# Kernel tuning notes

Hardware: AMD Instinct MI355X
Metric: run time of the kernel (lower is better)

The kernel has to match this reference:

```python
import jax, jax.numpy as jnp
import numpy as np
import math

B, S, D, H, L, V = 1, 2048, 512, 8, 2, 32000
DH = D // H
DFF = 2048
EPS = 1e-6
LN_EPS = 1e-5


def setup_inputs() -> dict:
    key = jax.random.key(0)
    ks = jax.random.split(key, 8)
    s = 0.02
    return {
        "input_ids": jax.random.randint(ks[0], (B, S), 0, V),
        "token_emb": jax.random.normal(ks[1], (V, D), jnp.float32) * s,
        "ln1_scale": jnp.ones((L, D), jnp.float32),
        "ln1_bias": jnp.zeros((L, D), jnp.float32),
        "qkv_w": jax.random.normal(ks[2], (L, D, 3 * D), jnp.float32) * s,
        "out_w": jax.random.normal(ks[3], (L, D, D), jnp.float32) * s,
        "ln2_scale": jnp.ones((L, D), jnp.float32),
        "ln2_bias": jnp.zeros((L, D), jnp.float32),
        "mlp_w1": jax.random.normal(ks[4], (L, D, DFF), jnp.float32) * s,
        "mlp_b1": jnp.zeros((L, DFF), jnp.float32),
        "mlp_w2": jax.random.normal(ks[5], (L, DFF, D), jnp.float32) * s,
        "mlp_b2": jnp.zeros((L, D), jnp.float32),
        "lnf_scale": jnp.ones((D,), jnp.float32),
        "lnf_bias": jnp.zeros((D,), jnp.float32),
        "head_w": jax.random.normal(ks[6], (D, V), jnp.float32) * s,
    }


def layernorm(x, scale, bias):
    mu = jnp.mean(x, axis=-1, keepdims=True)
    var = jnp.mean(jnp.square(x - mu), axis=-1, keepdims=True)
    return (x - mu) * jax.lax.rsqrt(var + LN_EPS) * scale + bias


def feature_map(x):
    return jax.nn.elu(x) + 1.0


def sinusoidal_pe(seq_len, d_model, dtype):
    pos = jnp.arange(seq_len, dtype=jnp.float32)[:, None]
    div = jnp.exp(jnp.arange(0, d_model, 2, dtype=jnp.float32) * (-math.log(10000.0) / d_model))
    pe = jnp.zeros((seq_len, d_model), jnp.float32)
    pe = pe.at[:, 0::2].set(jnp.sin(pos * div))
    pe = pe.at[:, 1::2].set(jnp.cos(pos * div))
    return pe.astype(dtype)


def linear_causal_attn(x, w_qkv, w_out):
    # x: (b, s, d)
    b, s, _ = x.shape
    qkv = x @ w_qkv  # (b, s, 3d)
    q, k, v = jnp.split(qkv, 3, axis=-1)
    split_heads = lambda t: t.reshape(b, s, H, DH).transpose(0, 2, 1, 3)  # (b,h,s,dh)
    q, k, v = split_heads(q), split_heads(k), split_heads(v)
    phi_q = feature_map(q)
    phi_k = feature_map(k)
    k_cum = jnp.cumsum(phi_k, axis=2)                          # (b,h,s,dh)
    kv = jnp.einsum('bhsi,bhsj->bhsij', phi_k, v)              # (b,h,s,dh,dh)
    kv_cum = jnp.cumsum(kv, axis=2)
    numer = jnp.einsum('bhsi,bhsij->bhsj', phi_q, kv_cum)      # (b,h,s,dh)
    denom = jnp.einsum('bhsi,bhsi->bhs', phi_q, k_cum) + EPS
    attn = numer / denom[..., None]
    attn = attn.transpose(0, 2, 1, 3).reshape(b, s, D)
    return attn @ w_out


def reference(input_ids, token_emb, ln1_scale, ln1_bias, qkv_w, out_w,
              ln2_scale, ln2_bias, mlp_w1, mlp_b1, mlp_w2, mlp_b2,
              lnf_scale, lnf_bias, head_w):
    tok = token_emb[input_ids]                 # (b, s, d)
    pos = sinusoidal_pe(input_ids.shape[1], D, tok.dtype)[None]
    x = tok + pos
    for l in range(L):
        a = linear_causal_attn(layernorm(x, ln1_scale[l], ln1_bias[l]), qkv_w[l], out_w[l])
        x = x + a
        h = layernorm(x, ln2_scale[l], ln2_bias[l])
        h = jax.nn.gelu(h @ mlp_w1[l] + mlp_b1[l], approximate=False) @ mlp_w2[l] + mlp_b2[l]
        x = x + h
    x = layernorm(x, lnf_scale, lnf_bias)
    logits = x @ head_w                        # (b, s, vocab)
    return logits
```

## Files before the change

### kernel.cpp

```cpp
#include <hip/hip_runtime.h>
#include <cstdint>

typedef unsigned short u16;
typedef __bf16 bf16x8 __attribute__((ext_vector_type(8)));
typedef float f32x4 __attribute__((ext_vector_type(4)));

#define DEV __device__ __forceinline__

DEV u16 f2bf(float f) {
  union { float f; unsigned u; } v; v.f = f;
  unsigned u = v.u;
  u += 0x7FFFu + ((u >> 16) & 1u);
  return (u16)(u >> 16);
}
DEV float bf2f(u16 u) {
  union { unsigned u; float f; } v; v.u = ((unsigned)u) << 16;
  return v.f;
}

DEV void load16(const u16* g, u16* l) {
  __builtin_amdgcn_global_load_lds(
      (const __attribute__((address_space(1))) unsigned int*)(const void*)g,
      (__attribute__((address_space(3))) unsigned int*)l, 16, 0, 0);
}

__global__ __launch_bounds__(256) void prep_kernel(
    const float* __restrict__ qkvw, const float* __restrict__ outw,
    const float* __restrict__ w1, const float* __restrict__ w2,
    const float* __restrict__ hw, u16* __restrict__ wq_t, u16* __restrict__ wo_t,
    u16* __restrict__ w1_t, u16* __restrict__ w2_t, u16* __restrict__ wh_t,
    const int* __restrict__ ids, const float* __restrict__ emb,
    const float* __restrict__ sc, const float* __restrict__ bi,
    float* __restrict__ x, u16* __restrict__ xn) {
  int b = blockIdx.x;
  __shared__ float t[64][65];
  if (b >= 5536) {
    int lane = threadIdx.x & 63, wave = threadIdx.x >> 6;
    int row = (b - 5536) * 4 + wave;
    int id = ids[row];
    float v[8];
#pragma unroll
    for (int i = 0; i < 8; ++i) {
      int c = lane + i * 64;
      float tk = emb[(size_t)id * 512 + c];
      int dp = c & ~1;
      float dv = expf((float)dp * (-9.210340371976184f / 512.0f));
      float ang = (float)row * dv;
      float pe = (c & 1) ? cosf(ang) : sinf(ang);
      v[i] = tk + pe;
      x[(size_t)row * 512 + c] = v[i];
    }
    float s = 0.f;
#pragma unroll
    for (int i = 0; i < 8; ++i) s += v[i];
#pragma unroll
    for (int m = 32; m; m >>= 1) s += __shfl_xor(s, m, 64);
    float mu = s * (1.0f / 512.0f);
    float var = 0.f;
#pragma unroll
    for (int i = 0; i < 8; ++i) { float d = v[i] - mu; var += d * d; }
#pragma unroll
    for (int m = 32; m; m >>= 1) var += __shfl_xor(var, m, 64);
    float rs = rsqrtf(var * (1.0f / 512.0f) + 1e-5f);
    u16* orow = xn + (size_t)row * 512;
#pragma unroll
    for (int i = 0; i < 8; ++i) {
      int c = lane + i * 64;
      orow[c] = f2bf((v[i] - mu) * rs * sc[c] + bi[c]);
    }
    return;
  }
  const float* in; u16* out; int K, N, nx, ky;
  if (b < 384)       { int z = b / 192, r = b % 192; nx = r % 24; ky = r / 24;
                       in = qkvw + (size_t)z * 786432; out = wq_t + (size_t)z * 786432; N = 1536; K = 512; }
  else if (b < 512)  { int tt = b - 384, z = tt / 64, r = tt % 64; nx = r % 8; ky = r / 8;
                       in = outw + (size_t)z * 262144; out = wo_t + (size_t)z * 262144; N = 512; K = 512; }
  else if (b < 1024) { int tt = b - 512, z = tt / 256, r = tt % 256; nx = r % 32; ky = r / 32;
                       in = w1 + (size_t)z * 1048576; out = w1_t + (size_t)z * 1048576; N = 2048; K = 512; }
  else if (b < 1536) { int tt = b - 1024, z = tt / 256, r = tt % 256; nx = r % 8; ky = r / 8;
                       in = w2 + (size_t)z * 1048576; out = w2_t + (size_t)z * 1048576; N = 512; K = 2048; }
  else               { int tt = b - 1536; nx = tt % 500; ky = tt / 500;
                       in = hw; out = wh_t; N = 32000; K = 512; }
  int n0 = nx * 64, k0 = ky * 64;
  for (int e = threadIdx.x; e < 4096; e += 256) {
    int r = e >> 6, c = e & 63;
    t[r][c] = in[(size_t)(k0 + r) * N + n0 + c];
  }
  __syncthreads();
  for (int e = threadIdx.x; e < 4096; e += 256) {
    int r = e >> 6, c = e & 63;
    out[(size_t)(n0 + r) * K + k0 + c] = f2bf(t[c][r]);
  }
}

__global__ __launch_bounds__(256) void reduce_ln(const float* __restrict__ part, int nz,
    const float* __restrict__ bias, float* __restrict__ x,
    const float* __restrict__ sc, const float* __restrict__ bi, u16* __restrict__ xn) {
  int lane = threadIdx.x & 63, wave = threadIdx.x >> 6;
  int row = blockIdx.x * 4 + wave;
  float* xr = x + (size_t)row * 512;
  float v[8];
#pragma unroll
  for (int i = 0; i < 8; ++i) v[i] = xr[lane + i * 64];
  if (bias) {
#pragma unroll
    for (int i = 0; i < 8; ++i) v[i] += bias[lane + i * 64];
  }
  for (int z = 0; z < nz; ++z) {
    const float* pz = part + (size_t)z * 1048576 + (size_t)row * 512;
#pragma unroll
    for (int i = 0; i < 8; ++i) v[i] += pz[lane + i * 64];
  }
#pragma unroll
  for (int i = 0; i < 8; ++i) xr[lane + i * 64] = v[i];
  float s = 0.f;
#pragma unroll
  for (int i = 0; i < 8; ++i) s += v[i];
#pragma unroll
  for (int m = 32; m; m >>= 1) s += __shfl_xor(s, m, 64);
  float mu = s * (1.0f / 512.0f);
  float var = 0.f;
#pragma unroll
  for (int i = 0; i < 8; ++i) { float d = v[i] - mu; var += d * d; }
#pragma unroll
  for (int m = 32; m; m >>= 1) var += __shfl_xor(var, m, 64);
  float rs = rsqrtf(var * (1.0f / 512.0f) + 1e-5f);
  u16* orow = xn + (size_t)row * 512;
#pragma unroll
  for (int i = 0; i < 8; ++i) {
    int c = lane + i * 64;
    orow[c] = f2bf((v[i] - mu) * rs * sc[c] + bi[c]);
  }
}

__global__ __launch_bounds__(256) void attn_intra(const u16* __restrict__ pq,
    const u16* __restrict__ pk, const u16* __restrict__ pv,
    float* __restrict__ numer, float* __restrict__ denom,
    float* __restrict__ KVc, float* __restrict__ Ksc) {
  int c = blockIdx.x, h = blockIdx.y;
  int s0 = c * 128;
  __shared__ u16 kl[128 * 72];
  __shared__ u16 kT[64 * 136];
  __shared__ u16 vT[64 * 136];
  __shared__ u16 P[128 * 136];
  int tid = threadIdx.x, lane = tid & 63, w = tid >> 6;
  int fr = lane & 15, kb = lane >> 4, rg = lane >> 4;
  const size_t base = ((size_t)h * 2048 + s0) * 64;

  for (int e = tid; e < 1024; e += 256) {
    int r = e >> 3, c8 = (e & 7) * 8;
    bf16x8 kv = *(const bf16x8*)&pk[base + r * 64 + c8];
    bf16x8 vv = *(const bf16x8*)&pv[base + r * 64 + c8];
    *(bf16x8*)&kl[r * 72 + c8] = kv;
#pragma unroll
    for (int tt = 0; tt < 8; ++tt) {
      kT[(c8 + tt) * 136 + r] = ((const u16*)&kv)[tt];
      vT[(c8 + tt) * 136 + r] = ((const u16*)&vv)[tt];
    }
  }
  int fiA = w, fiB = 7 - w;
  const u16* qA = pq + base + (size_t)(fiA * 16 + fr) * 64 + kb * 8;
  const u16* qB = pq + base + (size_t)(fiB * 16 + fr) * 64 + kb * 8;
  bf16x8 aQ0a = *(const bf16x8*)qA, aQ1a = *(const bf16x8*)(qA + 32);
  bf16x8 aQ0b = *(const bf16x8*)qB, aQ1b = *(const bf16x8*)(qB + 32);
  __syncthreads();

#pragma unroll
  for (int ph = 0; ph < 2; ++ph) {
    int fi = ph ? fiB : fiA;
    bf16x8 aQ0 = ph ? aQ0b : aQ0a, aQ1 = ph ? aQ1b : aQ1a;
    f32x4 dsum = {0.f, 0.f, 0.f, 0.f};
    for (int fj = 0; fj <= fi; ++fj) {
      f32x4 s4 = {0.f, 0.f, 0.f, 0.f};
      bf16x8 b0 = *(const bf16x8*)&kl[(fj * 16 + fr) * 72 + kb * 8];
      bf16x8 b1 = *(const bf16x8*)&kl[(fj * 16 + fr) * 72 + kb * 8 + 32];
      s4 = __builtin_amdgcn_mfma_f32_16x16x32_bf16(aQ0, b0, s4, 0, 0, 0);
      s4 = __builtin_amdgcn_mfma_f32_16x16x32_bf16(aQ1, b1, s4, 0, 0, 0);
      int colL = fj * 16 + fr;
#pragma unroll
      for (int rr = 0; rr < 4; ++rr) {
        int rowL = fi * 16 + rg * 4 + rr;
        float mv = (colL <= rowL) ? s4[rr] : 0.f;
        dsum[rr] += mv;
        P[rowL * 136 + colL] = f2bf(mv);
      }
    }
    if ((fi & 1) == 0) {
      int colL = (fi + 1) * 16 + fr;
#pragma unroll
      for (int rr = 0; rr < 4; ++rr) P[(fi * 16 + rg * 4 + rr) * 136 + colL] = 0;
    }
#pragma unroll
    for (int rr = 0; rr < 4; ++rr) {
      float v = dsum[rr];
      v += __shfl_xor(v, 1, 16); v += __shfl_xor(v, 2, 16);
      v += __shfl_xor(v, 4, 16); v += __shfl_xor(v, 8, 16);
      if (fr == 0) denom[(size_t)h * 2048 + s0 + fi * 16 + rg * 4 + rr] = v;
    }
  }
  __syncthreads();

#pragma unroll
  for (int ph = 0; ph < 2; ++ph) {
    int fi = ph ? fiB : fiA;
    int ktmax = (fi + 2) >> 1;
    f32x4 o0 = {0,0,0,0}, o1 = {0,0,0,0}, o2 = {0,0,0,0}, o3 = {0,0,0,0};
    for (int kt = 0; kt < ktmax; ++kt) {
      bf16x8 aP = *(const bf16x8*)&P[(fi * 16 + fr) * 136 + kt * 32 + kb * 8];
      o0 = __builtin_amdgcn_mfma_f32_16x16x32_bf16(aP, *(const bf16x8*)&vT[(0 * 16 + fr) * 136 + kt * 32 + kb * 8], o0, 0, 0, 0);
      o1 = __builtin_amdgcn_mfma_f32_16x16x32_bf16(aP, *(const bf16x8*)&vT[(1 * 16 + fr) * 136 + kt * 32 + kb * 8], o1, 0, 0, 0);
      o2 = __builtin_amdgcn_mfma_f32_16x16x32_bf16(aP, *(const bf16x8*)&vT[(2 * 16 + fr) * 136 + kt * 32 + kb * 8], o2, 0, 0, 0);
      o3 = __builtin_amdgcn_mfma_f32_16x16x32_bf16(aP, *(const bf16x8*)&vT[(3 * 16 + fr) * 136 + kt * 32 + kb * 8], o3, 0, 0, 0);
    }
#pragma unroll
    for (int rr = 0; rr < 4; ++rr) {
      size_t rb = base + (size_t)(fi * 16 + rg * 4 + rr) * 64;
      numer[rb + 0 + fr]  = o0[rr];
      numer[rb + 16 + fr] = o1[rr];
      numer[rb + 32 + fr] = o2[rr];
      numer[rb + 48 + fr] = o3[rr];
    }
  }

  {
    f32x4 k0 = {0,0,0,0}, k1 = {0,0,0,0}, k2 = {0,0,0,0}, k3 = {0,0,0,0};
    for (int kt = 0; kt < 4; ++kt) {
      bf16x8 aK = *(const bf16x8*)&kT[(w * 16 + fr) * 136 + kt * 32 + kb * 8];
      k0 = __builtin_amdgcn_mfma_f32_16x16x32_bf16(aK, *(const bf16x8*)&vT[(0 * 16 + fr) * 136 + kt * 32 + kb * 8], k0, 0, 0, 0);
      k1 = __builtin_amdgcn_mfma_f32_16x16x32_bf16(aK, *(const bf16x8*)&vT[(1 * 16 + fr) * 136 + kt * 32 + kb * 8], k1, 0, 0, 0);
      k2 = __builtin_amdgcn_mfma_f32_16x16x32_bf16(aK, *(const bf16x8*)&vT[(2 * 16 + fr) * 136 + kt * 32 + kb * 8], k2, 0, 0, 0);
      k3 = __builtin_amdgcn_mfma_f32_16x16x32_bf16(aK, *(const bf16x8*)&vT[(3 * 16 + fr) * 136 + kt * 32 + kb * 8], k3, 0, 0, 0);
    }
    float* kvb = KVc + ((size_t)h * 16 + c) * 4096;
#pragma unroll
    for (int rr = 0; rr < 4; ++rr) {
      int row = w * 16 + rg * 4 + rr;
      kvb[row * 64 + 0 + fr]  = k0[rr];
      kvb[row * 64 + 16 + fr] = k1[rr];
      kvb[row * 64 + 32 + fr] = k2[rr];
      kvb[row * 64 + 48 + fr] = k3[rr];
    }
  }
  if (tid < 64) {
    float s = 0.f;
    for (int t8 = 0; t8 < 16; ++t8) {
      bf16x8 kv = *(const bf16x8*)&kT[tid * 136 + t8 * 8];
#pragma unroll
      for (int tt = 0; tt < 8; ++tt) s += bf2f(((const u16*)&kv)[tt]);
    }
    Ksc[((size_t)h * 16 + c) * 64 + tid] = s;
  }
}

__global__ __launch_bounds__(256) void attn_inter(const u16* __restrict__ pq,
    const float* __restrict__ numer, const float* __restrict__ denom,
    const float* __restrict__ KVc, const float* __restrict__ Ksc,
    u16* __restrict__ attn) {
  int c = blockIdx.x, h = blockIdx.y;
  int s0 = c * 128;
  __shared__ float KVp[4096];
  __shared__ float Kp[64];
  __shared__ float ql[128 * 64];
  int tid = threadIdx.x;
  for (int e = tid; e < 1024; e += 256) {
    f32x4 a = {0.f, 0.f, 0.f, 0.f};
    for (int cp = 0; cp < c; ++cp)
      a += *(const f32x4*)&KVc[((size_t)h * 16 + cp) * 4096 + e * 4];
    *(f32x4*)&KVp[e * 4] = a;
  }
  if (tid < 64) {
    float a = 0.f;
    for (int cp = 0; cp < c; ++cp) a += Ksc[((size_t)h * 16 + cp) * 64 + tid];
    Kp[tid] = a;
  }
  for (int e = tid; e < 1024; e += 256) {
    bf16x8 q8 = *(const bf16x8*)&pq[((size_t)h * 2048 + s0) * 64 + e * 8];
#pragma unroll
    for (int tt = 0; tt < 8; ++tt) ql[e * 8 + tt] = bf2f(((const u16*)&q8)[tt]);
  }
  __syncthreads();
  int s = tid >> 1, half = tid & 1;
  float num[32];
  {
    const float* np_ = numer + ((size_t)h * 2048 + s0 + s) * 64 + half * 32;
#pragma unroll
    for (int i = 0; i < 8; ++i) *(f32x4*)&num[i * 4] = *(const f32x4*)&np_[i * 4];
  }
  float den = denom[(size_t)h * 2048 + s0 + s] + 1e-6f;
  for (int i = 0; i < 64; ++i) {
    float qv = ql[s * 64 + i];
    den += qv * Kp[i];
    const f32x4* kv = (const f32x4*)&KVp[i * 64 + half * 32];
#pragma unroll
    for (int j4 = 0; j4 < 8; ++j4) {
      f32x4 kvv = kv[j4];
#pragma unroll
      for (int t = 0; t < 4; ++t) num[j4 * 4 + t] += qv * kvv[t];
    }
  }
  float inv = 1.f / den;
  u16* op = attn + (size_t)(s0 + s) * 512 + h * 64 + half * 32;
#pragma unroll
  for (int j = 0; j < 32; ++j) op[j] = f2bf(num[j] * inv);
}

template <int EPI>
__global__ __launch_bounds__(512, 2) void gemm_bt(const u16* __restrict__ A,
    const u16* __restrict__ B, float* __restrict__ outF, u16* __restrict__ outB,
    const float* __restrict__ bias, int M, int N, int K, int Ksplit) {
  __shared__ u16 lds[32768];
  int tid = threadIdx.x, lane = tid & 63, w = tid >> 6;
  int f = blockIdx.x + gridDim.x * blockIdx.y;
  int m0 = (f & 15) << 7, n0 = (f >> 4) << 7;
  int wr = w >> 2, wc = w & 3;
  int fr = lane & 15, kb = lane >> 4;
  int z = blockIdx.z;
  int kbeg = z * Ksplit;
  int KT = Ksplit >> 6;

  auto stage = [&](int d, int u, int k0) {
    int t = u & 1;
    int row = t * 64 + w * 8 + (lane >> 3);
    int slot = (lane & 7) ^ ((lane >> 3) & 7);
    const u16* g = (u < 2 ? A + (size_t)(m0 + row) * K : B + (size_t)(n0 + row) * K)
                   + k0 + slot * 8;
    int dst = (u < 2 ? d * 8192 : 16384 + d * 8192) + t * 4096 + w * 512;
    load16(g, &lds[dst]);
  };
  auto rdA = [&](int d, int i, int kk) {
    int row = wr * 64 + i * 16 + fr;
    return *(const bf16x8*)&lds[d * 8192 + row * 64 + ((((kk << 2) | kb) ^ (fr & 7)) << 3)];
  };
  auto rdB = [&](int d, int j, int kk) {
    int row = wc * 32 + j * 16 + fr;
    return *(const bf16x8*)&lds[16384 + d * 8192 + row * 64 + ((((kk << 2) | kb) ^ (fr & 7)) << 3)];
  };

  f32x4 acc[4][2];
#pragma unroll
  for (int i = 0; i < 4; ++i)
#pragma unroll
    for (int j = 0; j < 2; ++j) acc[i][j] = (f32x4){0.f, 0.f, 0.f, 0.f};

#pragma unroll 1
  for (int u = 0; u < 4; ++u) stage(0, u, kbeg);
  __syncthreads();

  for (int t = 0; t < KT; ++t) {
    int d = t & 1, e = d ^ 1;
    int k1 = kbeg + ((t + 1) << 6);
    bool pre = (t + 1) < KT;
    bf16x8 aF[4], bF[2];
    if (pre) { stage(e, 0, k1); stage(e, 1, k1); }
#pragma unroll
    for (int i = 0; i < 4; ++i) aF[i] = rdA(d, i, 0);
#pragma unroll
    for (int j = 0; j < 2; ++j) bF[j] = rdB(d, j, 0);
    __builtin_amdgcn_s_setprio(1);
#pragma unroll
    for (int i = 0; i < 4; ++i)
#pragma unroll
      for (int j = 0; j < 2; ++j)
        acc[i][j] = __builtin_amdgcn_mfma_f32_16x16x32_bf16(aF[i], bF[j], acc[i][j], 0, 0, 0);
    __builtin_amdgcn_s_setprio(0);
    __builtin_amdgcn_sched_barrier(0);
    if (pre) { stage(e, 2, k1); stage(e, 3, k1); }
#pragma unroll
    for (int i = 0; i < 4; ++i) aF[i] = rdA(d, i, 1);
#pragma unroll
    for (int j = 0; j < 2; ++j) bF[j] = rdB(d, j, 1);
    __builtin_amdgcn_s_setprio(1);
#pragma unroll
    for (int i = 0; i < 4; ++i)
#pragma unroll
      for (int j = 0; j < 2; ++j)
        acc[i][j] = __builtin_amdgcn_mfma_f32_16x16x32_bf16(aF[i], bF[j], acc[i][j], 0, 0, 0);
    __builtin_amdgcn_s_setprio(0);
    __syncthreads();
  }

  int rq = lane >> 4;
#pragma unroll
  for (int i = 0; i < 4; ++i) {
#pragma unroll
    for (int j = 0; j < 2; ++j) {
      int col = n0 + wc * 32 + j * 16 + fr;
#pragma unroll
      for (int r = 0; r < 4; ++r) {
        int row = m0 + wr * 64 + i * 16 + rq * 4 + r;
        size_t o = (size_t)row * N + col;
        float vacc = acc[i][j][r];
        if (EPI == 2) {
          float t = vacc + bias[col];
          outB[o] = f2bf(0.5f * t * (1.f + erff(t * 0.70710678118654752f)));
        } else if (EPI == 4) {
          int part = col >> 9, d = col & 511, h = d >> 6, dh = d & 63;
          float wv = (part == 2) ? vacc : (vacc > 0.f ? vacc + 1.f : expf(vacc));
          outB[(size_t)part * 1048576 + (((size_t)h * 2048 + row) * 64 + dh)] = f2bf(wv);
        } else {
          outF[(size_t)z * 1048576 + o] = vacc;
        }
      }
    }
  }
}

__global__ __launch_bounds__(512, 2) void gemm256(const u16* __restrict__ A,
    const u16* __restrict__ B, float* __restrict__ C, int M, int N, int K) {
  __shared__ u16 lds[65536];
  int tid = threadIdx.x, lane = tid & 63, w = tid >> 6;
  int f = blockIdx.x;
  {
    int nwg = gridDim.x;
    int q = nwg >> 3;
    f = (f & 7) * q + (f >> 3);
  }
  int m0 = (f & 7) << 8;
  int n0 = (f >> 3) << 8;
  int wr = w >> 2, wc = w & 3;
  int fr = lane & 15, kb = lane >> 4;

  auto stage = [&](int d, int u, int k0) {
    int us = u & 3;
    int row = us * 64 + w * 8 + (lane >> 3);
    int slot = (lane & 7) ^ ((lane >> 3) & 7);
    const u16* g = (u < 4 ? A + (size_t)(m0 + row) * K : B + (size_t)(n0 + row) * K)
                   + k0 + slot * 8;
    int dst = (u < 4 ? d * 16384 : 32768 + d * 16384) + us * 4096 + w * 512;
    load16(g, &lds[dst]);
  };
  auto rdA = [&](int d, int i, int kk) {
    int row = wr * 128 + i * 16 + fr;
    return *(const bf16x8*)&lds[d * 16384 + row * 64 + ((((kk << 2) | kb) ^ (fr & 7)) << 3)];
  };
  auto rdB = [&](int d, int j, int kk) {
    int row = wc * 64 + j * 16 + fr;
    return *(const bf16x8*)&lds[32768 + d * 16384 + row * 64 + ((((kk << 2) | kb) ^ (fr & 7)) << 3)];
  };

  f32x4 acc[8][4];
#pragma unroll
  for (int i = 0; i < 8; ++i)
#pragma unroll
    for (int j = 0; j < 4; ++j) acc[i][j] = (f32x4){0.f, 0.f, 0.f, 0.f};

  int KT = K >> 6;
#pragma unroll 1
  for (int u = 0; u < 8; ++u) stage(0, u, 0);
  __syncthreads();

  for (int t = 0; t < KT; ++t) {
    int d = t & 1, e = d ^ 1;
    int k1 = (t + 1) << 6;
    bool pre = (t + 1) < KT;
    bf16x8 aF[4][2], bF[4][2];
    if (pre) { stage(e, 0, k1); stage(e, 1, k1); }
#pragma unroll
    for (int i = 0; i < 4; ++i) { aF[i][0] = rdA(d, i, 0); aF[i][1] = rdA(d, i, 1); }
#pragma unroll
    for (int j = 0; j < 2; ++j) { bF[j][0] = rdB(d, j, 0); bF[j][1] = rdB(d, j, 1); }
    __builtin_amdgcn_s_setprio(1);
#pragma unroll
    for (int i = 0; i < 4; ++i)
#pragma unroll
      for (int j = 0; j < 2; ++j)
#pragma unroll
        for (int kk = 0; kk < 2; ++kk)
          acc[i][j] = __builtin_amdgcn_mfma_f32_16x16x32_bf16(aF[i][kk], bF[j][kk], acc[i][j], 0, 0, 0);
    __builtin_amdgcn_s_setprio(0);
    __builtin_amdgcn_sched_barrier(0);
    if (pre) { stage(e, 2, k1); stage(e, 3, k1); }
#pragma unroll
    for (int j = 2; j < 4; ++j) { bF[j][0] = rdB(d, j, 0); bF[j][1] = rdB(d, j, 1); }
    __builtin_amdgcn_s_setprio(1);
#pragma unroll
    for (int i = 0; i < 4; ++i)
#pragma unroll
      for (int j = 2; j < 4; ++j)
#pragma unroll
        for (int kk = 0; kk < 2; ++kk)
          acc[i][j] = __builtin_amdgcn_mfma_f32_16x16x32_bf16(aF[i][kk], bF[j][kk], acc[i][j], 0, 0, 0);
    __builtin_amdgcn_s_setprio(0);
    __builtin_amdgcn_sched_barrier(0);
    if (pre) { stage(e, 4, k1); stage(e, 5, k1); }
#pragma unroll
    for (int i = 0; i < 4; ++i) { aF[i][0] = rdA(d, i + 4, 0); aF[i][1] = rdA(d, i + 4, 1); }
    __builtin_amdgcn_s_setprio(1);
#pragma unroll
    for (int i = 0; i < 4; ++i)
#pragma unroll
      for (int j = 0; j < 2; ++j)
#pragma unroll
        for (int kk = 0; kk < 2; ++kk)
          acc[i + 4][j] = __builtin_amdgcn_mfma_f32_16x16x32_bf16(aF[i][kk], bF[j][kk], acc[i + 4][j], 0, 0, 0);
    __builtin_amdgcn_s_setprio(0);
    __builtin_amdgcn_sched_barrier(0);
    if (pre) { stage(e, 6, k1); stage(e, 7, k1); }
    __builtin_amdgcn_s_setprio(1);
#pragma unroll
    for (int i = 0; i < 4; ++i)
#pragma unroll
      for (int j = 2; j < 4; ++j)
#pragma unroll
        for (int kk = 0; kk < 2; ++kk)
          acc[i + 4][j] = __builtin_amdgcn_mfma_f32_16x16x32_bf16(aF[i][kk], bF[j][kk], acc[i + 4][j], 0, 0, 0);
    __builtin_amdgcn_s_setprio(0);
    __syncthreads();
  }

  int rq = lane >> 4;
#pragma unroll
  for (int i = 0; i < 8; ++i) {
#pragma unroll
    for (int j = 0; j < 4; ++j) {
      int col = n0 + wc * 64 + j * 16 + fr;
#pragma unroll
      for (int r = 0; r < 4; ++r) {
        int row = m0 + wr * 128 + i * 16 + rq * 4 + r;
        C[(size_t)row * N + col] = acc[i][j][r];
      }
    }
  }
}

extern "C" void kernel_launch(void* const* d_in, const int* in_sizes, int n_in,
                              void* d_out, int out_size, void* d_ws, size_t ws_size,
                              hipStream_t stream) {
  const int*   ids  = (const int*)d_in[0];
  const float* tok  = (const float*)d_in[1];
  const float* ln1s = (const float*)d_in[2];
  const float* ln1b = (const float*)d_in[3];
  const float* qkvw = (const float*)d_in[4];
  const float* outw = (const float*)d_in[5];
  const float* ln2s = (const float*)d_in[6];
  const float* ln2b = (const float*)d_in[7];
  const float* w1   = (const float*)d_in[8];
  const float* b1   = (const float*)d_in[9];
  const float* w2   = (const float*)d_in[10];
  const float* b2   = (const float*)d_in[11];
  const float* lnfs = (const float*)d_in[12];
  const float* lnfb = (const float*)d_in[13];
  const float* hw   = (const float*)d_in[14];
  float* out = (float*)d_out;

  char* ws = (char*)d_ws;
  size_t off = 0;
  auto carve = [&](size_t bytes) {
    char* p = ws + off;
    off = (off + bytes + 255) & ~(size_t)255;
    return p;
  };
  u16*   wq_t   = (u16*)carve(2ull * 1536 * 512 * 2);
  u16*   wo_t   = (u16*)carve(2ull * 512 * 512 * 2);
  u16*   w1_t   = (u16*)carve(2ull * 2048 * 512 * 2);
  u16*   w2_t   = (u16*)carve(2ull * 512 * 2048 * 2);
  u16*   wh_t   = (u16*)carve(32000ull * 512 * 2);
  float* x      = (float*)carve(2048ull * 512 * 4);
  u16*   xn     = (u16*)carve(2048ull * 512 * 2);
  u16*   phiAll = (u16*)carve(3ull * 8 * 2048 * 64 * 2);
  float* numer  = (float*)carve(8ull * 2048 * 64 * 4);
  float* denom  = (float*)carve(8ull * 2048 * 4);
  float* KVc    = (float*)carve(8ull * 16 * 4096 * 4);
  float* Ksc    = (float*)carve(8ull * 16 * 64 * 4);
  u16*   attn   = (u16*)carve(2048ull * 512 * 2);
  u16*   hmid   = (u16*)carve(2048ull * 2048 * 2);
  float* part   = (float*)carve(4ull * 2048 * 512 * 4);
  (void)ws_size; (void)in_sizes; (void)n_in; (void)out_size;

  u16* phiq = phiAll;
  u16* phik = phiAll + 1048576;
  u16* vbf  = phiAll + 2097152;

  prep_kernel<<<6048, 256, 0, stream>>>(qkvw, outw, w1, w2, hw,
                                        wq_t, wo_t, w1_t, w2_t, wh_t,
                                        ids, tok, ln1s, ln1b, x, xn);

  for (int l = 0; l < 2; ++l) {
    const u16* wq_l = wq_t + (size_t)l * 1536 * 512;
    const u16* wo_l = wo_t + (size_t)l * 512 * 512;
    const u16* w1_l = w1_t + (size_t)l * 2048 * 512;
    const u16* w2_l = w2_t + (size_t)l * 512 * 2048;
    const float* nls = (l == 0) ? ln1s + 512 : lnfs;
    const float* nlb = (l == 0) ? ln1b + 512 : lnfb;

    gemm_bt<4><<<dim3(12, 16), 512, 0, stream>>>(xn, wq_l, nullptr, phiAll, nullptr,
                                                 2048, 1536, 512, 512);
    attn_intra<<<dim3(16, 8), 256, 0, stream>>>(phiq, phik, vbf, numer, denom, KVc, Ksc);
    attn_inter<<<dim3(16, 8), 256, 0, stream>>>(phiq, numer, denom, KVc, Ksc, attn);
    gemm_bt<5><<<dim3(4, 16, 2), 512, 0, stream>>>(attn, wo_l, part, nullptr, nullptr,
                                                   2048, 512, 512, 256);
    reduce_ln<<<512, 256, 0, stream>>>(part, 2, nullptr, x, ln2s + l * 512, ln2b + l * 512, xn);
    gemm_bt<2><<<dim3(16, 16), 512, 0, stream>>>(xn, w1_l, nullptr, hmid, b1 + l * 2048,
                                                 2048, 2048, 512, 512);
    gemm_bt<5><<<dim3(4, 16, 4), 512, 0, stream>>>(hmid, w2_l, part, nullptr, nullptr,
                                                   2048, 512, 2048, 512);
    reduce_ln<<<512, 256, 0, stream>>>(part, 4, b2 + l * 512, x, nls, nlb, xn);
  }

  gemm256<<<1000, 512, 0, stream>>>(xn, wh_t, out, 2048, 32000, 512);
}
```

Measured before the change: 309.7 us.

## Fuse layernorm into GEMM prologue and residual add into GEMM epilogue

```diff
diff --git a/kernel.cpp b/kernel.cpp
--- a/kernel.cpp
+++ b/kernel.cpp
@@ -30,15 +30,13 @@
     const float* __restrict__ hw, u16* __restrict__ wq_t, u16* __restrict__ wo_t,
     u16* __restrict__ w1_t, u16* __restrict__ w2_t, u16* __restrict__ wh_t,
     const int* __restrict__ ids, const float* __restrict__ emb,
-    const float* __restrict__ sc, const float* __restrict__ bi,
-    float* __restrict__ x, u16* __restrict__ xn) {
+    float* __restrict__ x) {
   int b = blockIdx.x;
   __shared__ float t[64][65];
   if (b >= 5536) {
     int lane = threadIdx.x & 63, wave = threadIdx.x >> 6;
     int row = (b - 5536) * 4 + wave;
     int id = ids[row];
-    float v[8];
 #pragma unroll
     for (int i = 0; i < 8; ++i) {
       int c = lane + i * 64;
@@ -47,26 +45,7 @@
       float dv = expf((float)dp * (-9.210340371976184f / 512.0f));
       float ang = (float)row * dv;
       float pe = (c & 1) ? cosf(ang) : sinf(ang);
-      v[i] = tk + pe;
-      x[(size_t)row * 512 + c] = v[i];
-    }
-    float s = 0.f;
-#pragma unroll
-    for (int i = 0; i < 8; ++i) s += v[i];
-#pragma unroll
-    for (int m = 32; m; m >>= 1) s += __shfl_xor(s, m, 64);
-    float mu = s * (1.0f / 512.0f);
-    float var = 0.f;
-#pragma unroll
-    for (int i = 0; i < 8; ++i) { float d = v[i] - mu; var += d * d; }
-#pragma unroll
-    for (int m = 32; m; m >>= 1) var += __shfl_xor(var, m, 64);
-    float rs = rsqrtf(var * (1.0f / 512.0f) + 1e-5f);
-    u16* orow = xn + (size_t)row * 512;
-#pragma unroll
-    for (int i = 0; i < 8; ++i) {
-      int c = lane + i * 64;
-      orow[c] = f2bf((v[i] - mu) * rs * sc[c] + bi[c]);
+      x[(size_t)row * 512 + c] = tk + pe;
     }
     return;
   }
@@ -93,26 +72,14 @@
   }
 }
 
-__global__ __launch_bounds__(256) void reduce_ln(const float* __restrict__ part, int nz,
-    const float* __restrict__ bias, float* __restrict__ x,
-    const float* __restrict__ sc, const float* __restrict__ bi, u16* __restrict__ xn) {
+__global__ __launch_bounds__(256) void ln_kernel(const float* __restrict__ x,
+    const float* __restrict__ sc, const float* __restrict__ bi, u16* __restrict__ out) {
   int lane = threadIdx.x & 63, wave = threadIdx.x >> 6;
   int row = blockIdx.x * 4 + wave;
-  float* xr = x + (size_t)row * 512;
+  const float* xr = x + (size_t)row * 512;
   float v[8];
 #pragma unroll
   for (int i = 0; i < 8; ++i) v[i] = xr[lane + i * 64];
-  if (bias) {
-#pragma unroll
-    for (int i = 0; i < 8; ++i) v[i] += bias[lane + i * 64];
-  }
-  for (int z = 0; z < nz; ++z) {
-    const float* pz = part + (size_t)z * 1048576 + (size_t)row * 512;
-#pragma unroll
-    for (int i = 0; i < 8; ++i) v[i] += pz[lane + i * 64];
-  }
-#pragma unroll
-  for (int i = 0; i < 8; ++i) xr[lane + i * 64] = v[i];
   float s = 0.f;
 #pragma unroll
   for (int i = 0; i < 8; ++i) s += v[i];
@@ -125,7 +92,7 @@
 #pragma unroll
   for (int m = 32; m; m >>= 1) var += __shfl_xor(var, m, 64);
   float rs = rsqrtf(var * (1.0f / 512.0f) + 1e-5f);
-  u16* orow = xn + (size_t)row * 512;
+  u16* orow = out + (size_t)row * 512;
 #pragma unroll
   for (int i = 0; i < 8; ++i) {
     int c = lane + i * 64;
@@ -305,60 +272,168 @@
 }
 
 template <int EPI>
-__global__ __launch_bounds__(512, 2) void gemm_bt(const u16* __restrict__ A,
-    const u16* __restrict__ B, float* __restrict__ outF, u16* __restrict__ outB,
-    const float* __restrict__ bias, int M, int N, int K, int Ksplit) {
-  __shared__ u16 lds[32768];
+__global__ __launch_bounds__(256, 2) void gemm_ln(const float* __restrict__ x,
+    const float* __restrict__ sc, const float* __restrict__ bi,
+    const u16* __restrict__ B, u16* __restrict__ outB,
+    const float* __restrict__ bias, int N) {
+  __shared__ u16 lds[40960];
   int tid = threadIdx.x, lane = tid & 63, w = tid >> 6;
-  int f = blockIdx.x + gridDim.x * blockIdx.y;
-  int m0 = (f & 15) << 7, n0 = (f >> 4) << 7;
-  int wr = w >> 2, wc = w & 3;
+  int n0 = blockIdx.x << 6, m0 = blockIdx.y << 6;
+  int wr = w >> 1, wc = w & 1;
   int fr = lane & 15, kb = lane >> 4;
-  int z = blockIdx.z;
-  int kbeg = z * Ksplit;
-  int KT = Ksplit >> 6;
+
+  auto stageB = [&](int d, int u, int k0) {
+    int row = u * 32 + w * 8 + (lane >> 3);
+    int slot = (lane & 7) ^ ((lane >> 3) & 7);
+    const u16* g = B + (size_t)(n0 + row) * 512 + k0 + slot * 8;
+    int dst = 32768 + d * 4096 + u * 2048 + w * 512;
+    load16(g, &lds[dst]);
+  };
+  stageB(0, 0, 0); stageB(0, 1, 0);
+
+  {
+    int row = tid >> 2, ct = tid & 3;
+    const float* xr = x + (size_t)(m0 + row) * 512 + ct * 128;
+    float sum = 0.f, sq = 0.f;
+#pragma unroll
+    for (int g = 0; g < 32; ++g) {
+      f32x4 v = *(const f32x4*)(xr + g * 4);
+#pragma unroll
+      for (int e = 0; e < 4; ++e) { sum += v[e]; sq += v[e] * v[e]; }
+    }
+    sum += __shfl_xor(sum, 1, 64); sum += __shfl_xor(sum, 2, 64);
+    sq  += __shfl_xor(sq, 1, 64);  sq  += __shfl_xor(sq, 2, 64);
+    float mu = sum * (1.f / 512.f);
+    float rs = rsqrtf(sq * (1.f / 512.f) - mu * mu + 1e-5f);
+#pragma unroll
+    for (int g = 0; g < 16; ++g) {
+      int c = ct * 128 + g * 8;
+      f32x4 a0 = *(const f32x4*)(xr + g * 8);
+      f32x4 a1 = *(const f32x4*)(xr + g * 8 + 4);
+      f32x4 s0 = *(const f32x4*)(sc + c);
+      f32x4 s1 = *(const f32x4*)(sc + c + 4);
+      f32x4 c0 = *(const f32x4*)(bi + c);
+      f32x4 c1 = *(const f32x4*)(bi + c + 4);
+      u16 tmp[8];
+#pragma unroll
+      for (int e = 0; e < 4; ++e) tmp[e] = f2bf((a0[e] - mu) * rs * s0[e] + c0[e]);
+#pragma unroll
+      for (int e = 0; e < 4; ++e) tmp[4 + e] = f2bf((a1[e] - mu) * rs * s1[e] + c1[e]);
+      int slot = (ct * 16 + g) ^ (row & 7);
+      *(int4*)&lds[row * 512 + slot * 8] = *(const int4*)tmp;
+    }
+  }
+  __syncthreads();
+
+  f32x4 acc[2][2];
+#pragma unroll
+  for (int i = 0; i < 2; ++i)
+#pragma unroll
+    for (int j = 0; j < 2; ++j) acc[i][j] = (f32x4){0.f, 0.f, 0.f, 0.f};
+
+  for (int t = 0; t < 8; ++t) {
+    int d = t & 1, e = d ^ 1;
+    if (t < 7) { stageB(e, 0, (t + 1) * 64); stageB(e, 1, (t + 1) * 64); }
+    bf16x8 aF[2][2], bF[2][2];
+#pragma unroll
+    for (int i = 0; i < 2; ++i)
+#pragma unroll
+      for (int kk = 0; kk < 2; ++kk)
+        aF[i][kk] = *(const bf16x8*)&lds[(wr * 32 + i * 16 + fr) * 512 +
+                                         (((t * 8 + kk * 4 + kb) ^ (fr & 7)) << 3)];
+#pragma unroll
+    for (int j = 0; j < 2; ++j)
+#pragma unroll
+      for (int kk = 0; kk < 2; ++kk)
+        bF[j][kk] = *(const bf16x8*)&lds[32768 + d * 4096 + (wc * 32 + j * 16 + fr) * 64 +
+                                         ((((kk << 2) | kb) ^ (fr & 7)) << 3)];
+    __builtin_amdgcn_s_setprio(1);
+#pragma unroll
+    for (int i = 0; i < 2; ++i)
+#pragma unroll
+      for (int j = 0; j < 2; ++j)
+#pragma unroll
+        for (int kk = 0; kk < 2; ++kk)
+          acc[i][j] = __builtin_amdgcn_mfma_f32_16x16x32_bf16(aF[i][kk], bF[j][kk], acc[i][j], 0, 0, 0);
+    __builtin_amdgcn_s_setprio(0);
+    __syncthreads();
+  }
+
+  int rq = lane >> 4;
+#pragma unroll
+  for (int i = 0; i < 2; ++i) {
+#pragma unroll
+    for (int j = 0; j < 2; ++j) {
+      int col = n0 + wc * 32 + j * 16 + fr;
+#pragma unroll
+      for (int r = 0; r < 4; ++r) {
+        int row = m0 + wr * 32 + i * 16 + rq * 4 + r;
+        float vacc = acc[i][j][r];
+        if (EPI == 2) {
+          float t = vacc + bias[col];
+          outB[(size_t)row * N + col] = f2bf(0.5f * t * (1.f + erff(t * 0.70710678118654752f)));
+        } else {
+          int part = col >> 9, d = col & 511, h = d >> 6, dh = d & 63;
+          float wv = (part == 2) ? vacc : (vacc > 0.f ? vacc + 1.f : expf(vacc));
+          outB[(size_t)part * 1048576 + (((size_t)h * 2048 + row) * 64 + dh)] = f2bf(wv);
+        }
+      }
+    }
+  }
+}
+
+template <bool BIAS>
+__global__ __launch_bounds__(256, 4) void gemm64(const u16* __restrict__ A,
+    const u16* __restrict__ B, float* __restrict__ x,
+    const float* __restrict__ bias, int K) {
+  __shared__ u16 lds[16384];
+  int tid = threadIdx.x, lane = tid & 63, w = tid >> 6;
+  int n0 = blockIdx.x << 6, m0 = blockIdx.y << 6;
+  int wr = w >> 1, wc = w & 1;
+  int fr = lane & 15, kb = lane >> 4;
+  int KT = K >> 6;
 
   auto stage = [&](int d, int u, int k0) {
     int t = u & 1;
-    int row = t * 64 + w * 8 + (lane >> 3);
+    int row = t * 32 + w * 8 + (lane >> 3);
     int slot = (lane & 7) ^ ((lane >> 3) & 7);
     const u16* g = (u < 2 ? A + (size_t)(m0 + row) * K : B + (size_t)(n0 + row) * K)
                    + k0 + slot * 8;
-    int dst = (u < 2 ? d * 8192 : 16384 + d * 8192) + t * 4096 + w * 512;
+    int dst = (u < 2 ? d * 4096 : 8192 + d * 4096) + t * 2048 + w * 512;
     load16(g, &lds[dst]);
   };
   auto rdA = [&](int d, int i, int kk) {
-    int row = wr * 64 + i * 16 + fr;
-    return *(const bf16x8*)&lds[d * 8192 + row * 64 + ((((kk << 2) | kb) ^ (fr & 7)) << 3)];
+    int row = wr * 32 + i * 16 + fr;
+    return *(const bf16x8*)&lds[d * 4096 + row * 64 + ((((kk << 2) | kb) ^ (fr & 7)) << 3)];
   };
   auto rdB = [&](int d, int j, int kk) {
     int row = wc * 32 + j * 16 + fr;
-    return *(const bf16x8*)&lds[16384 + d * 8192 + row * 64 + ((((kk << 2) | kb) ^ (fr & 7)) << 3)];
-  };
-
-  f32x4 acc[4][2];
-#pragma unroll
-  for (int i = 0; i < 4; ++i)
+    return *(const bf16x8*)&lds[8192 + d * 4096 + row * 64 + ((((kk << 2) | kb) ^ (fr & 7)) << 3)];
+  };
+
+  f32x4 acc[2][2];
+#pragma unroll
+  for (int i = 0; i < 2; ++i)
 #pragma unroll
     for (int j = 0; j < 2; ++j) acc[i][j] = (f32x4){0.f, 0.f, 0.f, 0.f};
 
 #pragma unroll 1
-  for (int u = 0; u < 4; ++u) stage(0, u, kbeg);
+  for (int u = 0; u < 4; ++u) stage(0, u, 0);
   __syncthreads();
 
   for (int t = 0; t < KT; ++t) {
     int d = t & 1, e = d ^ 1;
-    int k1 = kbeg + ((t + 1) << 6);
+    int k1 = (t + 1) << 6;
     bool pre = (t + 1) < KT;
-    bf16x8 aF[4], bF[2];
+    bf16x8 aF[2], bF[2];
     if (pre) { stage(e, 0, k1); stage(e, 1, k1); }
 #pragma unroll
-    for (int i = 0; i < 4; ++i) aF[i] = rdA(d, i, 0);
+    for (int i = 0; i < 2; ++i) aF[i] = rdA(d, i, 0);
 #pragma unroll
     for (int j = 0; j < 2; ++j) bF[j] = rdB(d, j, 0);
     __builtin_amdgcn_s_setprio(1);
 #pragma unroll
-    for (int i = 0; i < 4; ++i)
+    for (int i = 0; i < 2; ++i)
 #pragma unroll
       for (int j = 0; j < 2; ++j)
         acc[i][j] = __builtin_amdgcn_mfma_f32_16x16x32_bf16(aF[i], bF[j], acc[i][j], 0, 0, 0);
@@ -366,12 +441,12 @@
     __builtin_amdgcn_sched_barrier(0);
     if (pre) { stage(e, 2, k1); stage(e, 3, k1); }
 #pragma unroll
-    for (int i = 0; i < 4; ++i) aF[i] = rdA(d, i, 1);
+    for (int i = 0; i < 2; ++i) aF[i] = rdA(d, i, 1);
 #pragma unroll
     for (int j = 0; j < 2; ++j) bF[j] = rdB(d, j, 1);
     __builtin_amdgcn_s_setprio(1);
 #pragma unroll
-    for (int i = 0; i < 4; ++i)
+    for (int i = 0; i < 2; ++i)
 #pragma unroll
       for (int j = 0; j < 2; ++j)
         acc[i][j] = __builtin_amdgcn_mfma_f32_16x16x32_bf16(aF[i], bF[j], acc[i][j], 0, 0, 0);
@@ -381,25 +456,17 @@
 
   int rq = lane >> 4;
 #pragma unroll
-  for (int i = 0; i < 4; ++i) {
+  for (int i = 0; i < 2; ++i) {
 #pragma unroll
     for (int j = 0; j < 2; ++j) {
       int col = n0 + wc * 32 + j * 16 + fr;
 #pragma unroll
       for (int r = 0; r < 4; ++r) {
-        int row = m0 + wr * 64 + i * 16 + rq * 4 + r;
-        size_t o = (size_t)row * N + col;
-        float vacc = acc[i][j][r];
-        if (EPI == 2) {
-          float t = vacc + bias[col];
-          outB[o] = f2bf(0.5f * t * (1.f + erff(t * 0.70710678118654752f)));
-        } else if (EPI == 4) {
-          int part = col >> 9, d = col & 511, h = d >> 6, dh = d & 63;
-          float wv = (part == 2) ? vacc : (vacc > 0.f ? vacc + 1.f : expf(vacc));
-          outB[(size_t)part * 1048576 + (((size_t)h * 2048 + row) * 64 + dh)] = f2bf(wv);
-        } else {
-          outF[(size_t)z * 1048576 + o] = vacc;
-        }
+        int row = m0 + wr * 32 + i * 16 + rq * 4 + r;
+        size_t o = (size_t)row * 512 + col;
+        float add = acc[i][j][r];
+        if (BIAS) add += bias[col];
+        x[o] += add;
       }
     }
   }
@@ -564,7 +631,6 @@
   float* Ksc    = (float*)carve(8ull * 16 * 64 * 4);
   u16*   attn   = (u16*)carve(2048ull * 512 * 2);
   u16*   hmid   = (u16*)carve(2048ull * 2048 * 2);
-  float* part   = (float*)carve(4ull * 2048 * 512 * 4);
   (void)ws_size; (void)in_sizes; (void)n_in; (void)out_size;
 
   u16* phiq = phiAll;
@@ -573,29 +639,24 @@
 
   prep_kernel<<<6048, 256, 0, stream>>>(qkvw, outw, w1, w2, hw,
                                         wq_t, wo_t, w1_t, w2_t, wh_t,
-                                        ids, tok, ln1s, ln1b, x, xn);
+                                        ids, tok, x);
 
   for (int l = 0; l < 2; ++l) {
     const u16* wq_l = wq_t + (size_t)l * 1536 * 512;
     const u16* wo_l = wo_t + (size_t)l * 512 * 512;
     const u16* w1_l = w1_t + (size_t)l * 2048 * 512;
     const u16* w2_l = w2_t + (size_t)l * 512 * 2048;
-    const float* nls = (l == 0) ? ln1s + 512 : lnfs;
-    const float* nlb = (l == 0) ? ln1b + 512 : lnfb;
-
-    gemm_bt<4><<<dim3(12, 16), 512, 0, stream>>>(xn, wq_l, nullptr, phiAll, nullptr,
-                                                 2048, 1536, 512, 512);
+
+    gemm_ln<4><<<dim3(24, 32), 256, 0, stream>>>(x, ln1s + l * 512, ln1b + l * 512,
+                                                 wq_l, phiAll, nullptr, 1536);
     attn_intra<<<dim3(16, 8), 256, 0, stream>>>(phiq, phik, vbf, numer, denom, KVc, Ksc);
     attn_inter<<<dim3(16, 8), 256, 0, stream>>>(phiq, numer, denom, KVc, Ksc, attn);
-    gemm_bt<5><<<dim3(4, 16, 2), 512, 0, stream>>>(attn, wo_l, part, nullptr, nullptr,
-                                                   2048, 512, 512, 256);
-    reduce_ln<<<512, 256, 0, stream>>>(part, 2, nullptr, x, ln2s + l * 512, ln2b + l * 512, xn);
-    gemm_bt<2><<<dim3(16, 16), 512, 0, stream>>>(xn, w1_l, nullptr, hmid, b1 + l * 2048,
-                                                 2048, 2048, 512, 512);
-    gemm_bt<5><<<dim3(4, 16, 4), 512, 0, stream>>>(hmid, w2_l, part, nullptr, nullptr,
-                                                   2048, 512, 2048, 512);
-    reduce_ln<<<512, 256, 0, stream>>>(part, 4, b2 + l * 512, x, nls, nlb, xn);
-  }
-
+    gemm64<false><<<dim3(8, 32), 256, 0, stream>>>(attn, wo_l, x, nullptr, 512);
+    gemm_ln<2><<<dim3(32, 32), 256, 0, stream>>>(x, ln2s + l * 512, ln2b + l * 512,
+                                                 w1_l, hmid, b1 + l * 2048, 2048);
+    gemm64<true><<<dim3(8, 32), 256, 0, stream>>>(hmid, w2_l, x, b2 + l * 512, 2048);
+  }
+
+  ln_kernel<<<512, 256, 0, stream>>>(x, lnfs, lnfb, xn);
   gemm256<<<1000, 512, 0, stream>>>(xn, wh_t, out, 2048, 32000, 512);
 }
```

New measurement: 473.2 us. 52.8% more time.
